# Kernel optimization log

Hardware: AMD Instinct MI355X
Metric: run time of the kernel (lower is better)

## Reference

```python
import jax, jax.numpy as jnp
import numpy as np
import math


def _dct2_mat(N):
    # DCT-II matrix, norm=None convention of torch_dct: X[k] = 2*sum_n x[n]*cos(pi*(2n+1)*k/(2N))
    n = np.arange(N)
    k = n[:, None]
    C = 2.0 * np.cos(np.pi * (2 * n[None, :] + 1) * k / (2 * N))
    return jnp.asarray(C, dtype=jnp.float32)


def setup_inputs() -> dict:
    key = jax.random.key(0)
    k1, k2, k3 = jax.random.split(key, 3)
    B, H, W = 128, 256, 256
    thresh = int(H / (2 * math.sqrt(2)))  # 90
    x = jax.random.normal(k1, (B, 3, H, W), dtype=jnp.float32)
    w = jax.random.normal(k2, (1, thresh), dtype=jnp.float32) * 0.05
    b = jax.random.normal(k3, (1,), dtype=jnp.float32) * 0.05
    return {"x": x, "w": w, "b": b}


def reference(x, w, b):
    B, C, H, W = x.shape
    Ch = _dct2_mat(H)
    Cw = _dct2_mat(W)
    # dct_2d: DCT-II along last two dims
    xd = jnp.einsum('bchw,kw->bchk', x, Cw)
    xd = jnp.einsum('bchk,jh->bcjk', xd, Ch)
    xd = jax.lax.stop_gradient(xd)  # original does x.detach() inside get_fft_feature
    gray = 0.2989 * xd[:, 0] + 0.587 * xd[:, 1] + 0.114 * xd[:, 2]  # [B,H,W]
    F = jnp.fft.fft2(gray, axes=(-2, -1))
    re = F.real + 1e-8  # original adds epsilon to both real and imag parts
    im = F.imag + 1e-8
    mag = jnp.log(jnp.sqrt(re * re + im * im + 1e-10) + 1e-10)
    mag = jnp.fft.fftshift(mag, axes=(-2, -1))  # quadrant-swap `shift` == fftshift for even dims
    # radial binning (static integer radii, as in azimuthalAverage)
    yy, xx = np.indices([H, W])
    r = np.sqrt((xx - H / 2) ** 2 + (yy - W / 2) ** 2).astype(np.int32).ravel()
    nbins = int(r.max()) + 1
    nr = jnp.asarray(np.bincount(r, minlength=nbins).astype(np.float32))
    rj = jnp.asarray(r)
    tbin = jax.vmap(lambda m: jax.ops.segment_sum(m, rj, num_segments=nbins))(mag.reshape(B, -1))
    prof = tbin / (nr + 1e-10)  # [B, nbins]
    prof = prof[:, 1:-2]  # azimuthalAverage returns radial_prof[1:-2]
    mn = jnp.min(prof, axis=1, keepdims=True)
    mx = jnp.max(prof, axis=1, keepdims=True)
    out = (prof - mn) / (mx - mn)
    out = jnp.where(jnp.isnan(out), 0.0, out)
    thresh = w.shape[1]
    feat = out[:, -thresh:]  # [B, thresh]
    return feat @ w.T + b  # [B, 1]
```

## Files before the change

### kernel.cpp

```cpp
#include <hip/hip_runtime.h>
#include <math.h>

#define NBINS 182
#define NB 128

typedef unsigned short u16;
typedef __attribute__((ext_vector_type(8))) short short8;
typedef __attribute__((ext_vector_type(4))) float f32x4;

__device__ __forceinline__ u16 f2bf(float f) {
    union { float f; unsigned u; } v; v.f = f;
    unsigned r = v.u + 0x7FFF + ((v.u >> 16) & 1);
    return (u16)(r >> 16);
}
__device__ __forceinline__ float bf2f(u16 u) {
    union { unsigned u; float f; } v; v.u = ((unsigned)u) << 16;
    return v.f;
}
__device__ __forceinline__ short8 negbf(short8 v) {
    short8 r;
#pragma unroll
    for (int i = 0; i < 8; ++i) r[i] = v[i] ^ (short)0x8000;
    return r;
}

__device__ __forceinline__ int radial_bin(int dx, int dy) {
    int d2 = dx * dx + dy * dy;
    int bin = (int)sqrtf((float)d2);
    while ((bin + 1) * (bin + 1) <= d2) ++bin;
    while (bin * bin > d2) --bin;
    return bin;
}

__global__ __launch_bounds__(256) void prep(const float* __restrict__ x,
                                            u16* __restrict__ G,
                                            float* __restrict__ M_re,
                                            float* __restrict__ M_im,
                                            u16* __restrict__ A1,
                                            float* __restrict__ nrpart,
                                            float* __restrict__ tbin) {
    __shared__ double ctab[1024];
    __shared__ double stab[1024];
    __shared__ float s[NBINS];
    int blk = blockIdx.x;
    int t = threadIdx.x;

    if (blk < 256) {
        for (int i = t; i < 1024; i += 256) {
            double a = 3.14159265358979323846 * (double)i / 512.0;
            ctab[i] = cos(a);
            stab[i] = sin(a);
        }
        __syncthreads();
        int j = blk;
        int w = t;
        double re = 0.0, im = 0.0;
        int tw = 2 * w + 1;
        for (int k = 0; k < 256; ++k) {
            int e = (4 * j * k) & 1023;
            int m = (tw * k) & 1023;
            double cw = 2.0 * ctab[m];
            re += ctab[e] * cw;
            im -= stab[e] * cw;
        }
        M_re[j * 256 + w] = (float)re;
        M_im[j * 256 + w] = (float)im;
        A1[j * 256 + w] = f2bf((float)re);
        A1[(j + 256) * 256 + w] = f2bf((float)im);
    } else if (blk < 512) {
        int i = blk - 256;
        if (t < NBINS) s[t] = 0.0f;
        __syncthreads();
        int bin = radial_bin(t - 128, i - 128);
        atomicAdd(&s[bin], 1.0f);
        __syncthreads();
        if (t < NBINS) nrpart[i * NBINS + t] = s[t];
    } else if (blk < 544) {
        int idx = (blk - 512) * 256 + t;
        for (int i = idx; i < NB * NBINS; i += 32 * 256) tbin[i] = 0.0f;
    } else {
        int tid = (blk - 544) * 256 + t;
        for (int i = tid; i < 2097152; i += 262144) {
            int idx = i * 4;
            int b = idx >> 16;
            int rem = idx & 65535;
            const float* p = x + (size_t)b * 196608 + rem;
            float4 r = *(const float4*)p;
            float4 g = *(const float4*)(p + 65536);
            float4 bl = *(const float4*)(p + 131072);
            float g0 = 0.2989f * r.x + 0.587f * g.x + 0.114f * bl.x;
            float g1 = 0.2989f * r.y + 0.587f * g.y + 0.114f * bl.y;
            float g2 = 0.2989f * r.z + 0.587f * g.z + 0.114f * bl.z;
            float g3 = 0.2989f * r.w + 0.587f * g.w + 0.114f * bl.w;
            uint2 o;
            o.x = (unsigned)f2bf(g0) | ((unsigned)f2bf(g1) << 16);
            o.y = (unsigned)f2bf(g2) | ((unsigned)f2bf(g3) << 16);
            *(uint2*)(G + idx) = o;
        }
    }
}

__global__ __launch_bounds__(256) void s1(const u16* __restrict__ A1,
                                          const u16* __restrict__ G,
                                          u16* __restrict__ Tt_re,
                                          u16* __restrict__ Tt_im) {
    __shared__ u16 As[128 * 40];
    __shared__ u16 Bs[128 * 40];
    int b = blockIdx.z;
    int r0 = blockIdx.y * 128;
    int h0 = blockIdx.x * 128;
    int t = threadIdx.x;
    int lane = t & 63, wv = t >> 6;
    int wr = (wv >> 1) * 64;
    int wc = (wv & 1) * 64;
    int fr = lane & 15;
    int fk = (lane >> 4) << 3;

    f32x4 acc[4][4];
#pragma unroll
    for (int i = 0; i < 4; ++i)
#pragma unroll
        for (int j = 0; j < 4; ++j) acc[i][j] = (f32x4){0.f, 0.f, 0.f, 0.f};

    const u16* Ap = A1 + (size_t)r0 * 256;
    const u16* Gp = G + (size_t)b * 65536 + (size_t)h0 * 256;

    for (int kk = 0; kk < 256; kk += 32) {
#pragma unroll
        for (int c = t; c < 512; c += 256) {
            int row = c >> 2, off = (c & 3) << 3;
            *(uint4*)&As[row * 40 + off] =
                *(const uint4*)(Ap + (size_t)row * 256 + kk + off);
            *(uint4*)&Bs[row * 40 + off] =
                *(const uint4*)(Gp + (size_t)row * 256 + kk + off);
        }
        __syncthreads();
        short8 af[4], bfr[4];
#pragma unroll
        for (int i = 0; i < 4; ++i)
            af[i] = *(const short8*)&As[(wr + i * 16 + fr) * 40 + fk];
#pragma unroll
        for (int j = 0; j < 4; ++j)
            bfr[j] = *(const short8*)&Bs[(wc + j * 16 + fr) * 40 + fk];
#pragma unroll
        for (int i = 0; i < 4; ++i)
#pragma unroll
            for (int j = 0; j < 4; ++j)
                acc[i][j] = __builtin_amdgcn_mfma_f32_16x16x32_bf16(
                    af[i], bfr[j], acc[i][j], 0, 0, 0);
        __syncthreads();
    }

    u16* dst = ((r0 < 256) ? Tt_re : Tt_im) + (size_t)b * 65536
             + (size_t)(r0 & 255) * 256;
    int rq = (lane >> 4) << 2;
#pragma unroll
    for (int i = 0; i < 4; ++i)
#pragma unroll
        for (int j = 0; j < 4; ++j) {
            int col = h0 + wc + j * 16 + fr;
#pragma unroll
            for (int reg = 0; reg < 4; ++reg) {
                int row = wr + i * 16 + rq + reg;
                dst[(size_t)row * 256 + col] = f2bf(acc[i][j][reg]);
            }
        }
}

__global__ __launch_bounds__(256) void s2f(const u16* __restrict__ A1,
                                           const float* __restrict__ M_re,
                                           const u16* __restrict__ Tt_re,
                                           const u16* __restrict__ Tt_im,
                                           float* __restrict__ tbin) {
    __shared__ u16 Ar[64 * 40], Ai[64 * 40], Br[64 * 40], Bi[64 * 40];
    __shared__ float sbins[NBINS];
    __shared__ float sM[256];
    int blk = blockIdx.x;
    int t = threadIdx.x;

    if (blk >= 1024) {
        int b = blk - 1024;
        sM[t] = M_re[128 * 256 + t];
        __syncthreads();
        if (t > 128) return;
        const u16* pr = Tt_re + (size_t)b * 65536 + (size_t)t * 256;
        const u16* pi = Tt_im + (size_t)b * 65536 + (size_t)t * 256;
        float re = 0.0f, im = 0.0f;
        for (int h = 0; h < 256; h += 8) {
            uint4 vr = *(const uint4*)(pr + h);
            uint4 vi = *(const uint4*)(pi + h);
            unsigned wr[4] = {vr.x, vr.y, vr.z, vr.w};
            unsigned wi[4] = {vi.x, vi.y, vi.z, vi.w};
#pragma unroll
            for (int q = 0; q < 4; ++q) {
                re = fmaf(sM[h + 2 * q], bf2f((u16)(wr[q] & 0xffff)), re);
                re = fmaf(sM[h + 2 * q + 1], bf2f((u16)(wr[q] >> 16)), re);
                im = fmaf(sM[h + 2 * q], bf2f((u16)(wi[q] & 0xffff)), im);
                im = fmaf(sM[h + 2 * q + 1], bf2f((u16)(wi[q] >> 16)), im);
            }
        }
        re += 1e-8f; im += 1e-8f;
        float mag = logf(sqrtf(re * re + im * im + 1e-10f) + 1e-10f);
        float wj = (t == 0 || t == 128) ? 1.0f : 2.0f;
        int dx = (t < 128) ? t : t - 256;
        int bin = radial_bin(dx, -128);
        atomicAdd(&tbin[b * NBINS + bin], wj * mag);
        return;
    }

    int b = blk >> 3;
    int u0 = ((blk >> 2) & 1) * 64;
    int j0 = (blk & 3) * 64;
    int lane = t & 63, wv = t >> 6;
    int wu = (wv >> 1) * 32;
    int wj = (wv & 1) * 32;
    int fr = lane & 15;
    int fk = (lane >> 4) << 3;

    for (int i = t; i < NBINS; i += 256) sbins[i] = 0.0f;

    f32x4 accr[2][2], acci[2][2];
#pragma unroll
    for (int i = 0; i < 2; ++i)
#pragma unroll
        for (int j = 0; j < 2; ++j) {
            accr[i][j] = (f32x4){0.f, 0.f, 0.f, 0.f};
            acci[i][j] = (f32x4){0.f, 0.f, 0.f, 0.f};
        }

    const u16* Apr = A1 + (size_t)u0 * 256;
    const u16* Api = A1 + (size_t)(256 + u0) * 256;
    const u16* Tr = Tt_re + (size_t)b * 65536 + (size_t)j0 * 256;
    const u16* Ti = Tt_im + (size_t)b * 65536 + (size_t)j0 * 256;

    int lrow = t >> 2, loff = (t & 3) << 3;

    for (int kk = 0; kk < 256; kk += 32) {
        *(uint4*)&Ar[lrow * 40 + loff] =
            *(const uint4*)(Apr + (size_t)lrow * 256 + kk + loff);
        *(uint4*)&Ai[lrow * 40 + loff] =
            *(const uint4*)(Api + (size_t)lrow * 256 + kk + loff);
        *(uint4*)&Br[lrow * 40 + loff] =
            *(const uint4*)(Tr + (size_t)lrow * 256 + kk + loff);
        *(uint4*)&Bi[lrow * 40 + loff] =
            *(const uint4*)(Ti + (size_t)lrow * 256 + kk + loff);
        __syncthreads();
        short8 arf[2], aif[2], naif[2], brf[2], bif[2];
#pragma unroll
        for (int i = 0; i < 2; ++i) {
            arf[i] = *(const short8*)&Ar[(wu + i * 16 + fr) * 40 + fk];
            aif[i] = *(const short8*)&Ai[(wu + i * 16 + fr) * 40 + fk];
            naif[i] = negbf(aif[i]);
        }
#pragma unroll
        for (int j = 0; j < 2; ++j) {
            brf[j] = *(const short8*)&Br[(wj + j * 16 + fr) * 40 + fk];
            bif[j] = *(const short8*)&Bi[(wj + j * 16 + fr) * 40 + fk];
        }
#pragma unroll
        for (int i = 0; i < 2; ++i)
#pragma unroll
            for (int j = 0; j < 2; ++j) {
                accr[i][j] = __builtin_amdgcn_mfma_f32_16x16x32_bf16(
                    arf[i], brf[j], accr[i][j], 0, 0, 0);
                accr[i][j] = __builtin_amdgcn_mfma_f32_16x16x32_bf16(
                    naif[i], bif[j], accr[i][j], 0, 0, 0);
                acci[i][j] = __builtin_amdgcn_mfma_f32_16x16x32_bf16(
                    arf[i], bif[j], acci[i][j], 0, 0, 0);
                acci[i][j] = __builtin_amdgcn_mfma_f32_16x16x32_bf16(
                    aif[i], brf[j], acci[i][j], 0, 0, 0);
            }
        __syncthreads();
    }

    int rq = (lane >> 4) << 2;
#pragma unroll
    for (int i = 0; i < 2; ++i)
#pragma unroll
        for (int j = 0; j < 2; ++j) {
            int v = j0 + wj + j * 16 + fr;
            int dx = (v < 128) ? v : v - 256;
#pragma unroll
            for (int reg = 0; reg < 4; ++reg) {
                int u = u0 + wu + i * 16 + rq + reg;
                float wrow = (u == 0) ? 1.0f : 2.0f;
                int bin = radial_bin(dx, u);
                float re = accr[i][j][reg] + 1e-8f;
                float im = acci[i][j][reg] + 1e-8f;
                float mag = logf(sqrtf(re * re + im * im + 1e-10f) + 1e-10f);
                atomicAdd(&sbins[bin], wrow * mag);
            }
        }
    __syncthreads();
    for (int i = t; i < NBINS; i += 256)
        atomicAdd(&tbin[b * NBINS + i], sbins[i]);
}

__global__ __launch_bounds__(192) void finalize(const float* __restrict__ tbin,
                                                const float* __restrict__ nrpart,
                                                const float* __restrict__ w,
                                                const float* __restrict__ bias,
                                                float* __restrict__ out) {
    __shared__ float prof[NBINS];
    __shared__ float smn, smx, ssum;
    int b = blockIdx.x;
    int t = threadIdx.x;
    if (t < NBINS) {
        float nr = 0.0f;
        for (int i = 0; i < 256; ++i) nr += nrpart[i * NBINS + t];
        prof[t] = tbin[b * NBINS + t] / (nr + 1e-10f);
    }
    __syncthreads();
    if (t == 0) {
        float mn = prof[1], mx = prof[1];
        for (int i = 2; i <= 179; ++i) {
            float p = prof[i];
            mn = fminf(mn, p);
            mx = fmaxf(mx, p);
        }
        smn = mn; smx = mx; ssum = 0.0f;
    }
    __syncthreads();
    if (t < 90) {
        float denom = smx - smn;
        float v = (prof[90 + t] - smn) / denom;
        if (v != v) v = 0.0f;
        atomicAdd(&ssum, v * w[t]);
    }
    __syncthreads();
    if (t == 0) out[b] = ssum + bias[0];
}

extern "C" void kernel_launch(void* const* d_in, const int* in_sizes, int n_in,
                              void* d_out, int out_size, void* d_ws, size_t ws_size,
                              hipStream_t stream) {
    const float* x = (const float*)d_in[0];
    const float* w = (const float*)d_in[1];
    const float* bias = (const float*)d_in[2];
    float* out = (float*)d_out;

    float* M_re = (float*)d_ws;
    float* M_im = M_re + 65536;
    u16* A1 = (u16*)(M_im + 65536);
    u16* G = A1 + 131072;
    u16* Tt_re = G + (size_t)NB * 65536;
    u16* Tt_im = Tt_re + (size_t)NB * 65536;
    float* tbin = (float*)(Tt_im + (size_t)NB * 65536);
    float* nrpart = tbin + NB * NBINS;

    prep<<<1568, 256, 0, stream>>>(x, G, M_re, M_im, A1, nrpart, tbin);
    s1<<<dim3(2, 4, NB), 256, 0, stream>>>(A1, G, Tt_re, Tt_im);
    s2f<<<1152, 256, 0, stream>>>(A1, M_re, Tt_re, Tt_im, tbin);
    finalize<<<NB, 192, 0, stream>>>(tbin, nrpart, w, bias, out);
}
```

Baseline: 230.1 us.

## Stage s1 output through LDS, use fast log and sqrt bins, transpose nrpart

The s1 epilogue now writes accumulators into a shared-memory tile and stores them to global memory as coalesced 16-byte rows, replacing scattered 2-byte stores. The radial bin is computed directly with a float sqrt and no integer correction loops, and logf is replaced with __logf in the magnitude computation. The nrpart layout is transposed so finalize can sum it with contiguous float4 loads. Dropping the bin correction relies on sqrtf being exact for perfect squares, and __logf lowers accuracy slightly.

```diff
diff --git a/kernel.cpp b/kernel.cpp
--- a/kernel.cpp
+++ b/kernel.cpp
@@ -25,11 +25,7 @@
 }
 
 __device__ __forceinline__ int radial_bin(int dx, int dy) {
-    int d2 = dx * dx + dy * dy;
-    int bin = (int)sqrtf((float)d2);
-    while ((bin + 1) * (bin + 1) <= d2) ++bin;
-    while (bin * bin > d2) --bin;
-    return bin;
+    return (int)sqrtf((float)(dx * dx + dy * dy));
 }
 
 __global__ __launch_bounds__(256) void prep(const float* __restrict__ x,
@@ -74,7 +70,7 @@
         int bin = radial_bin(t - 128, i - 128);
         atomicAdd(&s[bin], 1.0f);
         __syncthreads();
-        if (t < NBINS) nrpart[i * NBINS + t] = s[t];
+        if (t < NBINS) nrpart[t * 256 + i] = s[t];
     } else if (blk < 544) {
         int idx = (blk - 512) * 256 + t;
         for (int i = idx; i < NB * NBINS; i += 32 * 256) tbin[i] = 0.0f;
@@ -106,6 +102,7 @@
                                           u16* __restrict__ Tt_im) {
     __shared__ u16 As[128 * 40];
     __shared__ u16 Bs[128 * 40];
+    __shared__ u16 Cs[64 * 136];
     int b = blockIdx.z;
     int r0 = blockIdx.y * 128;
     int h0 = blockIdx.x * 128;
@@ -151,20 +148,32 @@
         __syncthreads();
     }
 
-    u16* dst = ((r0 < 256) ? Tt_re : Tt_im) + (size_t)b * 65536
-             + (size_t)(r0 & 255) * 256;
+    u16* dstp = ((r0 < 256) ? Tt_re : Tt_im) + (size_t)b * 65536
+              + (size_t)(r0 & 255) * 256 + h0;
     int rq = (lane >> 4) << 2;
 #pragma unroll
-    for (int i = 0; i < 4; ++i)
-#pragma unroll
-        for (int j = 0; j < 4; ++j) {
-            int col = h0 + wc + j * 16 + fr;
-#pragma unroll
-            for (int reg = 0; reg < 4; ++reg) {
-                int row = wr + i * 16 + rq + reg;
-                dst[(size_t)row * 256 + col] = f2bf(acc[i][j][reg]);
-            }
-        }
+    for (int pass = 0; pass < 2; ++pass) {
+        if ((wr >> 6) == pass) {
+#pragma unroll
+            for (int i = 0; i < 4; ++i)
+#pragma unroll
+                for (int j = 0; j < 4; ++j) {
+                    int col = wc + j * 16 + fr;
+#pragma unroll
+                    for (int reg = 0; reg < 4; ++reg) {
+                        int lrow = i * 16 + rq + reg;
+                        Cs[lrow * 136 + col] = f2bf(acc[i][j][reg]);
+                    }
+                }
+        }
+        __syncthreads();
+        for (int idx = t; idx < 1024; idx += 256) {
+            int row = idx >> 4, k = idx & 15;
+            *(uint4*)(dstp + (size_t)(pass * 64 + row) * 256 + k * 8) =
+                *(const uint4*)&Cs[row * 136 + k * 8];
+        }
+        __syncthreads();
+    }
 }
 
 __global__ __launch_bounds__(256) void s2f(const u16* __restrict__ A1,
@@ -200,7 +209,7 @@
             }
         }
         re += 1e-8f; im += 1e-8f;
-        float mag = logf(sqrtf(re * re + im * im + 1e-10f) + 1e-10f);
+        float mag = __logf(sqrtf(re * re + im * im + 1e-10f) + 1e-10f);
         float wj = (t == 0 || t == 128) ? 1.0f : 2.0f;
         int dx = (t < 128) ? t : t - 256;
         int bin = radial_bin(dx, -128);
@@ -280,14 +289,15 @@
         for (int j = 0; j < 2; ++j) {
             int v = j0 + wj + j * 16 + fr;
             int dx = (v < 128) ? v : v - 256;
+            int dx2 = dx * dx;
 #pragma unroll
             for (int reg = 0; reg < 4; ++reg) {
                 int u = u0 + wu + i * 16 + rq + reg;
                 float wrow = (u == 0) ? 1.0f : 2.0f;
-                int bin = radial_bin(dx, u);
+                int bin = (int)sqrtf((float)(dx2 + u * u));
                 float re = accr[i][j][reg] + 1e-8f;
                 float im = acci[i][j][reg] + 1e-8f;
-                float mag = logf(sqrtf(re * re + im * im + 1e-10f) + 1e-10f);
+                float mag = __logf(sqrtf(re * re + im * im + 1e-10f) + 1e-10f);
                 atomicAdd(&sbins[bin], wrow * mag);
             }
         }
@@ -306,8 +316,13 @@
     int b = blockIdx.x;
     int t = threadIdx.x;
     if (t < NBINS) {
-        float nr = 0.0f;
-        for (int i = 0; i < 256; ++i) nr += nrpart[i * NBINS + t];
+        const float4* p = (const float4*)(nrpart + t * 256);
+        float4 a = {0.f, 0.f, 0.f, 0.f};
+        for (int i = 0; i < 64; ++i) {
+            float4 v = p[i];
+            a.x += v.x; a.y += v.y; a.z += v.z; a.w += v.w;
+        }
+        float nr = (a.x + a.y) + (a.z + a.w);
         prof[t] = tbin[b * NBINS + t] / (nr + 1e-10f);
     }
     __syncthreads();
```

Measured after the change: 233.4 us. About the same (+1.4%).

## Simplify radial bin, use fast log, widen gray conversion, transpose nrpart layout

Applied to the files above, without the earlier changes.

Several micro-optimizations at once. The radial bin drops its integer correction loops and relies on the float sqrt alone, and the magnitude log switches to the fast __logf intrinsic. The grayscale conversion now launches one thread per 8 pixels with wider 16-byte stores instead of a grid-stride loop, so prep gets a larger grid. The per-row radius counts are stored transposed so finalize can sum them with contiguous float4 reads. Both the bin shortcut and __logf may differ slightly from the exact results in edge cases.

```diff
diff --git a/kernel.cpp b/kernel.cpp
--- a/kernel.cpp
+++ b/kernel.cpp
@@ -25,11 +25,7 @@
 }
 
 __device__ __forceinline__ int radial_bin(int dx, int dy) {
-    int d2 = dx * dx + dy * dy;
-    int bin = (int)sqrtf((float)d2);
-    while ((bin + 1) * (bin + 1) <= d2) ++bin;
-    while (bin * bin > d2) --bin;
-    return bin;
+    return (int)sqrtf((float)(dx * dx + dy * dy));
 }
 
 __global__ __launch_bounds__(256) void prep(const float* __restrict__ x,
@@ -74,29 +70,32 @@
         int bin = radial_bin(t - 128, i - 128);
         atomicAdd(&s[bin], 1.0f);
         __syncthreads();
-        if (t < NBINS) nrpart[i * NBINS + t] = s[t];
+        if (t < NBINS) nrpart[t * 256 + i] = s[t];
     } else if (blk < 544) {
         int idx = (blk - 512) * 256 + t;
         for (int i = idx; i < NB * NBINS; i += 32 * 256) tbin[i] = 0.0f;
     } else {
         int tid = (blk - 544) * 256 + t;
-        for (int i = tid; i < 2097152; i += 262144) {
-            int idx = i * 4;
-            int b = idx >> 16;
-            int rem = idx & 65535;
-            const float* p = x + (size_t)b * 196608 + rem;
-            float4 r = *(const float4*)p;
-            float4 g = *(const float4*)(p + 65536);
-            float4 bl = *(const float4*)(p + 131072);
-            float g0 = 0.2989f * r.x + 0.587f * g.x + 0.114f * bl.x;
-            float g1 = 0.2989f * r.y + 0.587f * g.y + 0.114f * bl.y;
-            float g2 = 0.2989f * r.z + 0.587f * g.z + 0.114f * bl.z;
-            float g3 = 0.2989f * r.w + 0.587f * g.w + 0.114f * bl.w;
-            uint2 o;
-            o.x = (unsigned)f2bf(g0) | ((unsigned)f2bf(g1) << 16);
-            o.y = (unsigned)f2bf(g2) | ((unsigned)f2bf(g3) << 16);
-            *(uint2*)(G + idx) = o;
-        }
+        int idx = tid * 8;
+        int b = idx >> 16;
+        int rem = idx & 65535;
+        const float* p = x + (size_t)b * 196608 + rem;
+        float4 r0 = *(const float4*)p;
+        float4 r1 = *(const float4*)(p + 4);
+        float4 g0 = *(const float4*)(p + 65536);
+        float4 g1 = *(const float4*)(p + 65540);
+        float4 b0 = *(const float4*)(p + 131072);
+        float4 b1 = *(const float4*)(p + 131076);
+        uint4 o;
+        o.x = (unsigned)f2bf(0.2989f * r0.x + 0.587f * g0.x + 0.114f * b0.x)
+            | ((unsigned)f2bf(0.2989f * r0.y + 0.587f * g0.y + 0.114f * b0.y) << 16);
+        o.y = (unsigned)f2bf(0.2989f * r0.z + 0.587f * g0.z + 0.114f * b0.z)
+            | ((unsigned)f2bf(0.2989f * r0.w + 0.587f * g0.w + 0.114f * b0.w) << 16);
+        o.z = (unsigned)f2bf(0.2989f * r1.x + 0.587f * g1.x + 0.114f * b1.x)
+            | ((unsigned)f2bf(0.2989f * r1.y + 0.587f * g1.y + 0.114f * b1.y) << 16);
+        o.w = (unsigned)f2bf(0.2989f * r1.z + 0.587f * g1.z + 0.114f * b1.z)
+            | ((unsigned)f2bf(0.2989f * r1.w + 0.587f * g1.w + 0.114f * b1.w) << 16);
+        *(uint4*)(G + idx) = o;
     }
 }
 
@@ -200,7 +199,7 @@
             }
         }
         re += 1e-8f; im += 1e-8f;
-        float mag = logf(sqrtf(re * re + im * im + 1e-10f) + 1e-10f);
+        float mag = __logf(sqrtf(re * re + im * im + 1e-10f) + 1e-10f);
         float wj = (t == 0 || t == 128) ? 1.0f : 2.0f;
         int dx = (t < 128) ? t : t - 256;
         int bin = radial_bin(dx, -128);
@@ -280,14 +279,15 @@
         for (int j = 0; j < 2; ++j) {
             int v = j0 + wj + j * 16 + fr;
             int dx = (v < 128) ? v : v - 256;
+            int dx2 = dx * dx;
 #pragma unroll
             for (int reg = 0; reg < 4; ++reg) {
                 int u = u0 + wu + i * 16 + rq + reg;
                 float wrow = (u == 0) ? 1.0f : 2.0f;
-                int bin = radial_bin(dx, u);
+                int bin = (int)sqrtf((float)(dx2 + u * u));
                 float re = accr[i][j][reg] + 1e-8f;
                 float im = acci[i][j][reg] + 1e-8f;
-                float mag = logf(sqrtf(re * re + im * im + 1e-10f) + 1e-10f);
+                float mag = __logf(sqrtf(re * re + im * im + 1e-10f) + 1e-10f);
                 atomicAdd(&sbins[bin], wrow * mag);
             }
         }
@@ -306,8 +306,13 @@
     int b = blockIdx.x;
     int t = threadIdx.x;
     if (t < NBINS) {
-        float nr = 0.0f;
-        for (int i = 0; i < 256; ++i) nr += nrpart[i * NBINS + t];
+        const float4* p = (const float4*)(nrpart + t * 256);
+        float4 a = {0.f, 0.f, 0.f, 0.f};
+        for (int i = 0; i < 64; ++i) {
+            float4 v = p[i];
+            a.x += v.x; a.y += v.y; a.z += v.z; a.w += v.w;
+        }
+        float nr = (a.x + a.y) + (a.z + a.w);
         prof[t] = tbin[b * NBINS + t] / (nr + 1e-10f);
     }
     __syncthreads();
@@ -348,7 +353,7 @@
     float* tbin = (float*)(Tt_im + (size_t)NB * 65536);
     float* nrpart = tbin + NB * NBINS;
 
-    prep<<<1568, 256, 0, stream>>>(x, G, M_re, M_im, A1, nrpart, tbin);
+    prep<<<4640, 256, 0, stream>>>(x, G, M_re, M_im, A1, nrpart, tbin);
     s1<<<dim3(2, 4, NB), 256, 0, stream>>>(A1, G, Tt_re, Tt_im);
     s2f<<<1152, 256, 0, stream>>>(A1, M_re, Tt_re, Tt_im, tbin);
     finalize<<<NB, 192, 0, stream>>>(tbin, nrpart, w, bias, out);
```

Result: no change. 230.5 us (+0.2%).
